# Performance work log

Measured on AMD Instinct MI355X. Metric: run time of the kernel, lower is better.

The kernel has to match this reference:

```python
import jax, jax.numpy as jnp
import numpy as np

B, S, D_IN, D_OUT = 4, 4096, 768, 768

def setup_inputs() -> dict:
    key = jax.random.key(0)
    k1, k2, k3, k4 = jax.random.split(key, 4)
    x = jax.random.normal(k1, (B, S, D_IN), dtype=jnp.float32)
    # Stored as [d_in, d_out]; torch Linear computes x @ W.T with W [d_out, d_in],
    # which is equivalent to x @ W_here for a fresh random init.
    Wq = jax.random.normal(k2, (D_IN, D_OUT), dtype=jnp.float32) * (1.0 / np.sqrt(D_IN))
    Wk = jax.random.normal(k3, (D_IN, D_OUT), dtype=jnp.float32) * (1.0 / np.sqrt(D_IN))
    Wv = jax.random.normal(k4, (D_IN, D_OUT), dtype=jnp.float32) * (1.0 / np.sqrt(D_IN))
    return {"x": x, "Wq": Wq, "Wk": Wk, "Wv": Wv}

def reference(x, Wq, Wk, Wv):
    # x: [B, S, d_in]
    q = jnp.einsum('bsi,io->bso', x, Wq)  # [B, S, d_out]
    k = jnp.einsum('bsi,io->bso', x, Wk)
    v = jnp.einsum('bsi,io->bso', x, Wv)
    scale = 1.0 / jnp.sqrt(jnp.asarray(q.shape[-1], dtype=q.dtype))
    scores = jnp.einsum('bqd,bkd->bqk', q, k)  # [B, S, S]
    S_len = scores.shape[-1]
    causal = jnp.tril(jnp.ones((S_len, S_len), dtype=bool))  # True = keep
    scores = jnp.where(causal[None, :, :], scores, -jnp.inf)
    weights = jax.nn.softmax(scores * scale, axis=-1)
    # dropout p=0.0 -> identity
    return jnp.einsum('bqk,bkd->bqd', weights, v)
```

## Files before the change

kernel.cpp:

```cpp
#include <hip/hip_runtime.h>

typedef __attribute__((ext_vector_type(8))) short short8;
typedef __attribute__((ext_vector_type(4))) float f32x4;
typedef unsigned short u16;

#define MFMA_BF16 __builtin_amdgcn_mfma_f32_16x16x32_bf16
#define S_BARRIER()  asm volatile("s_barrier" ::: "memory")
#define WAIT_LGKM0() asm volatile("s_waitcnt lgkmcnt(0)" ::: "memory")
#define WAIT_VM(n)   asm volatile("s_waitcnt vmcnt(" #n ")" ::: "memory")

__device__ __forceinline__ u16 f2bf(float f) {
    unsigned int u = __builtin_bit_cast(unsigned int, f);
    u = (u + 0x7FFFu + ((u >> 16) & 1u)) >> 16;
    return (u16)u;
}

__device__ __forceinline__ void gl_lds16(const void* g, void* l) {
    __builtin_amdgcn_global_load_lds(
        (const __attribute__((address_space(1))) unsigned int*)g,
        (__attribute__((address_space(3))) unsigned int*)l, 16, 0, 0);
}

constexpr int D = 768;
constexpr int S = 4096;
constexpr float SCALE = 0.03608439182435161f;

__device__ __forceinline__ void tri_decode(int t, int& i, int& j) {
    i = (int)((sqrtf(8.0f * t + 1.0f) - 1.0f) * 0.5f);
    while ((i + 1) * (i + 2) / 2 <= t) ++i;
    while (i * (i + 1) / 2 > t) --i;
    j = t - i * (i + 1) / 2;
}

template<int NCH, int NT>
__device__ __forceinline__ void stageT(const u16* __restrict__ g, u16* lds, int kcol, int tid) {
    #pragma unroll
    for (int i = 0; i < NCH; ++i) {
        const int ch = i * NT + tid;
        const int row = ch >> 3, c = ch & 7;
        const int cs = c ^ (row & 7);
        gl_lds16(g + (size_t)row * 768 + kcol + cs * 8, lds + ch * 8);
    }
}
__device__ __forceinline__ short8 ldsfrag(const u16* p, int row, int ks, int lane) {
    const int cs = (ks * 4 + (lane >> 4)) ^ (row & 7);
    return *reinterpret_cast<const short8*>(p + row * 64 + cs * 8);
}

__global__ __launch_bounds__(256)
void conv_x(const float* __restrict__ x, u16* __restrict__ xb) {
    const size_t i = ((size_t)blockIdx.x * 256 + threadIdx.x) * 4;
    const float4 v = *reinterpret_cast<const float4*>(x + i);
    ushort4 o;
    o.x = f2bf(v.x); o.y = f2bf(v.y); o.z = f2bf(v.z); o.w = f2bf(v.w);
    *reinterpret_cast<ushort4*>(xb + i) = o;
}

__global__ __launch_bounds__(256)
void conv_wt(const float* __restrict__ Wq, const float* __restrict__ Wk,
             const float* __restrict__ Wv, u16* __restrict__ WT) {
    __shared__ float t[64][65];
    const int tid = threadIdx.x;
    const int k0 = blockIdx.x * 64, n0 = blockIdx.y * 64, z = blockIdx.z;
    const float* __restrict__ W = (z == 0) ? Wq : ((z == 1) ? Wk : Wv);
    #pragma unroll
    for (int i = 0; i < 4; ++i) {
        const int e = (i * 256 + tid) * 4;
        const int r = e >> 6, c = e & 63;
        const float4 v = *reinterpret_cast<const float4*>(W + (size_t)(k0 + r) * D + n0 + c);
        t[r][c] = v.x; t[r][c + 1] = v.y; t[r][c + 2] = v.z; t[r][c + 3] = v.w;
    }
    __syncthreads();
    u16* O = WT + (size_t)z * D * D;
    #pragma unroll
    for (int i = 0; i < 4; ++i) {
        const int e = (i * 256 + tid) * 4;
        const int n = e >> 6, kq = e & 63;
        ushort4 o;
        o.x = f2bf(t[kq + 0][n]); o.y = f2bf(t[kq + 1][n]);
        o.z = f2bf(t[kq + 2][n]); o.w = f2bf(t[kq + 3][n]);
        *reinterpret_cast<ushort4*>(O + (size_t)(n0 + n) * D + k0 + kq) = o;
    }
}

__global__ __launch_bounds__(256, 2)
void qkv_gemm(const u16* __restrict__ xb, const u16* __restrict__ WT,
              u16* __restrict__ qo, u16* __restrict__ ko, u16* __restrict__ vt)
{
    __shared__ u16 smem[40960];
    u16* sAb = smem;
    u16* sBb = smem + 16384;
    const int tid = threadIdx.x, lane = tid & 63, w = tid >> 6;
    const int wr = w >> 1, wn = w & 1;
    const int bm = blockIdx.x * 128;
    const u16* __restrict__ A = xb + (size_t)bm * 768;
    const u16* __restrict__ B = WT + (size_t)blockIdx.y * 192 * 768;

    f32x4 acc[4][6] = {};

    stageT<4,256>(A, sAb, 0, tid);          stageT<6,256>(B, sBb, 0, tid);
    stageT<4,256>(A, sAb + 8192, 64, tid);  stageT<6,256>(B, sBb + 12288, 64, tid);
    WAIT_VM(10); S_BARRIER();

    #pragma unroll 2
    for (int kt = 0; kt < 12; ++kt) {
        const int cur = kt & 1;
        const u16* pA = sAb + cur * 8192;
        const u16* pB = sBb + cur * 12288;
        short8 a0[4], b0[6], a1[4], b1[6];
        #pragma unroll
        for (int fr = 0; fr < 4; ++fr) a0[fr] = ldsfrag(pA, wr * 64 + fr * 16 + (lane & 15), 0, lane);
        #pragma unroll
        for (int fc = 0; fc < 6; ++fc) b0[fc] = ldsfrag(pB, wn * 96 + fc * 16 + (lane & 15), 0, lane);
        #pragma unroll
        for (int fr = 0; fr < 4; ++fr)
            #pragma unroll
            for (int fc = 0; fc < 6; ++fc)
                acc[fr][fc] = MFMA_BF16(a0[fr], b0[fc], acc[fr][fc], 0, 0, 0);
        #pragma unroll
        for (int fr = 0; fr < 4; ++fr) a1[fr] = ldsfrag(pA, wr * 64 + fr * 16 + (lane & 15), 1, lane);
        #pragma unroll
        for (int fc = 0; fc < 6; ++fc) b1[fc] = ldsfrag(pB, wn * 96 + fc * 16 + (lane & 15), 1, lane);
        WAIT_LGKM0(); S_BARRIER();
        if (kt < 10) { stageT<4,256>(A, sAb + cur * 8192, (kt + 2) * 64, tid);
                       stageT<6,256>(B, sBb + cur * 12288, (kt + 2) * 64, tid); }
        __builtin_amdgcn_s_setprio(1);
        #pragma unroll
        for (int fr = 0; fr < 4; ++fr)
            #pragma unroll
            for (int fc = 0; fc < 6; ++fc)
                acc[fr][fc] = MFMA_BF16(a1[fr], b1[fc], acc[fr][fc], 0, 0, 0);
        __builtin_amdgcn_s_setprio(0);
        if (kt < 10) { WAIT_VM(10); } else { WAIT_VM(0); }
        S_BARRIER();
    }

    const int z = blockIdx.y >> 2, nb = (blockIdx.y & 3) * 192;
    if (z == 2) {
        u16* sT = smem;
        #pragma unroll
        for (int fr = 0; fr < 4; ++fr)
            #pragma unroll
            for (int fc = 0; fc < 6; ++fc) {
                const int n  = wn * 96 + fc * 16 + (lane & 15);
                const int mb = wr * 64 + fr * 16 + (lane >> 4) * 4;
                ushort4 pk;
                pk.x = f2bf(acc[fr][fc][0]); pk.y = f2bf(acc[fr][fc][1]);
                pk.z = f2bf(acc[fr][fc][2]); pk.w = f2bf(acc[fr][fc][3]);
                *reinterpret_cast<ushort4*>(&sT[n * 128 + (mb ^ ((n & 7) << 3))]) = pk;
            }
        __syncthreads();
        const int batch = bm >> 12, s_in = bm & 4095;
        u16* __restrict__ vdst = vt + ((size_t)batch * 768 + nb) * 4096 + s_in;
        #pragma unroll
        for (int v = 0; v < 12; ++v) {
            const int ch = v * 256 + tid;
            const int dd = ch >> 4, sc = ch & 15;
            const short8 o = *reinterpret_cast<const short8*>(
                &sT[dd * 128 + ((sc * 8) ^ ((dd & 7) << 3))]);
            *reinterpret_cast<short8*>(vdst + (size_t)dd * 4096 + sc * 8) = o;
        }
    } else {
        u16* __restrict__ dst = (z == 0) ? qo : ko;
        #pragma unroll
        for (int fr = 0; fr < 4; ++fr)
            #pragma unroll
            for (int fc = 0; fc < 6; ++fc)
                #pragma unroll
                for (int r = 0; r < 4; ++r) {
                    const int m = bm + wr * 64 + fr * 16 + (lane >> 4) * 4 + r;
                    const int n = nb + wn * 96 + fc * 16 + (lane & 15);
                    dst[(size_t)m * 768 + n] = f2bf(acc[fr][fc][r]);
                }
    }
}

__global__ __launch_bounds__(256, 2)
void qkt_gemm(const u16* __restrict__ Qg, const u16* __restrict__ Kg,
              u16* __restrict__ Pp, float* __restrict__ Lp)
{
    __shared__ u16 smem[32768];
    const int tid = threadIdx.x, lane = tid & 63, w = tid >> 6;
    const int wr = w >> 1, wn = w & 1;
    const int bx = blockIdx.x;
    const int bxs = (bx & 7) * 66 + (bx >> 3);
    int ti, tj;
    tri_decode(bxs, ti, tj);
    const int b = blockIdx.y;
    const u16* __restrict__ A = Qg + ((size_t)b * S + ti * 128) * 768;
    const u16* __restrict__ B = Kg + ((size_t)b * S + tj * 128) * 768;

    f32x4 acc[4][4] = {};

    stageT<4,256>(A, smem, 0, tid);           stageT<4,256>(B, smem + 16384, 0, tid);
    stageT<4,256>(A, smem + 8192, 64, tid);   stageT<4,256>(B, smem + 24576, 64, tid);
    WAIT_VM(8); S_BARRIER();

    #pragma unroll 2
    for (int kt = 0; kt < 12; ++kt) {
        const int cur = kt & 1;
        const u16* pA = smem + cur * 8192;
        const u16* pB = smem + 16384 + cur * 8192;
        short8 a0[4], b0[4], a1[4], b1[4];
        #pragma unroll
        for (int fr = 0; fr < 4; ++fr) a0[fr] = ldsfrag(pA, wr * 64 + fr * 16 + (lane & 15), 0, lane);
        #pragma unroll
        for (int fc = 0; fc < 4; ++fc) b0[fc] = ldsfrag(pB, wn * 64 + fc * 16 + (lane & 15), 0, lane);
        #pragma unroll
        for (int fr = 0; fr < 4; ++fr)
            #pragma unroll
            for (int fc = 0; fc < 4; ++fc)
                acc[fr][fc] = MFMA_BF16(a0[fr], b0[fc], acc[fr][fc], 0, 0, 0);
        #pragma unroll
        for (int fr = 0; fr < 4; ++fr) a1[fr] = ldsfrag(pA, wr * 64 + fr * 16 + (lane & 15), 1, lane);
        #pragma unroll
        for (int fc = 0; fc < 4; ++fc) b1[fc] = ldsfrag(pB, wn * 64 + fc * 16 + (lane & 15), 1, lane);
        WAIT_LGKM0(); S_BARRIER();
        if (kt < 10) { stageT<4,256>(A, smem + cur * 8192, (kt + 2) * 64, tid);
                       stageT<4,256>(B, smem + 16384 + cur * 8192, (kt + 2) * 64, tid); }
        __builtin_amdgcn_s_setprio(1);
        #pragma unroll
        for (int fr = 0; fr < 4; ++fr)
            #pragma unroll
            for (int fc = 0; fc < 4; ++fc)
                acc[fr][fc] = MFMA_BF16(a1[fr], b1[fc], acc[fr][fc], 0, 0, 0);
        __builtin_amdgcn_s_setprio(0);
        if (kt < 10) { WAIT_VM(8); } else { WAIT_VM(0); }
        S_BARRIER();
    }

    u16* sC = smem;
    const bool diag = (ti == tj);
    #pragma unroll
    for (int fr = 0; fr < 4; ++fr)
        #pragma unroll
        for (int r = 0; r < 4; ++r) {
            const int ml = wr * 64 + fr * 16 + (lane >> 4) * 4 + r;
            const int gm = ti * 128 + ml;
            float rs = 0.0f;
            #pragma unroll
            for (int fc = 0; fc < 4; ++fc) {
                const int nl = wn * 64 + fc * 16 + (lane & 15);
                float p = __expf(acc[fr][fc][r] * SCALE - 10.0f);
                if (diag && (tj * 128 + nl) > gm) p = 0.0f;
                rs += p;
                sC[ml * 132 + nl] = f2bf(p);
            }
            rs += __shfl_xor(rs, 1);
            rs += __shfl_xor(rs, 2);
            rs += __shfl_xor(rs, 4);
            rs += __shfl_xor(rs, 8);
            if ((lane & 15) == 0)
                Lp[((size_t)b * 64 + tj * 2 + wn) * 4096 + gm] = rs;
        }
    __syncthreads();
    u16* __restrict__ tbase = Pp + ((size_t)b * 528 + (size_t)ti * (ti + 1) / 2 + tj) * 16384;
    #pragma unroll
    for (int v = 0; v < 8; ++v) {
        const int ch = v * 256 + tid;
        const int row = ch >> 4, c = ch & 15;
        const short8 o = *reinterpret_cast<const short8*>(&sC[row * 132 + c * 8]);
        *reinterpret_cast<short8*>(tbase + row * 128 + c * 8) = o;
    }
}

__global__ __launch_bounds__(256)
void reduce_l(const float* __restrict__ Lp, float* __restrict__ Li)
{
    const int row = blockIdx.x * 256 + threadIdx.x;
    const int b = row >> 12, r = row & 4095;
    const int jm = 2 * (r >> 7) + 1;
    float l = 0.0f;
    for (int j = 0; j <= jm; ++j)
        l += Lp[((size_t)b * 64 + j) * 4096 + r];
    Li[row] = 1.0f / l;
}

__global__ __launch_bounds__(256)
void pv_gemm(const u16* __restrict__ Pp, const u16* __restrict__ Vt,
             const float* __restrict__ Li, float* __restrict__ out)
{
    __shared__ u16 sV[2][192 * 64];
    __shared__ u16 sP[2][128 * 64];
    const int tid  = threadIdx.x;
    const int lane = tid & 63;
    const int wd   = tid >> 6;
    const int bid  = blockIdx.x;
    const int rank = (bid < 256) ? bid : 767 - bid;
    const int i    = rank >> 4;
    const int b    = (rank >> 2) & 3;
    const int dq   = rank & 3;
    const int q0   = i * 128, d0 = dq * 192;
    const int nkt  = 2 * i + 2;
    const u16* __restrict__ Pt  = Pp + ((size_t)b * 528 + (size_t)i * (i + 1) / 2) * 16384;
    const u16* __restrict__ vtb = Vt + ((size_t)b * D + d0) * S;

    f32x4 acc[8][3] = {};

    auto stage_v = [&](int buf, int kt) {
        #pragma unroll
        for (int n = 0; n < 6; ++n) {
            const int ch  = n * 256 + tid;
            const int row = ch >> 3;
            const int csw = (ch & 7) ^ (row & 7);
            gl_lds16(vtb + (size_t)row * S + kt * 64 + csw * 8, &sV[buf][ch * 8]);
        }
    };
    auto stage_p = [&](int buf, int kt) {
        const u16* base = Pt + (size_t)(kt >> 1) * 16384 + (kt & 1) * 64;
        #pragma unroll
        for (int n = 0; n < 4; ++n) {
            const int ch  = n * 256 + tid;
            const int row = ch >> 3;
            const int csw = (ch & 7) ^ (row & 7);
            gl_lds16(base + row * 128 + csw * 8, &sP[buf][ch * 8]);
        }
    };

    stage_v(0, 0); stage_p(0, 0);
    __syncthreads();
    int cur = 0;
    for (int kt = 0; kt < nkt; ++kt) {
        if (kt + 1 < nkt) { stage_v(cur ^ 1, kt + 1); stage_p(cur ^ 1, kt + 1); }
        #pragma unroll
        for (int ks = 0; ks < 2; ++ks) {
            short8 a[8];
            #pragma unroll
            for (int fr = 0; fr < 8; ++fr) {
                const int row = fr * 16 + (lane & 15);
                const int cch = (ks * 4 + (lane >> 4)) ^ (row & 7);
                a[fr] = *reinterpret_cast<const short8*>(&sP[cur][row * 64 + cch * 8]);
            }
            #pragma unroll
            for (int fc = 0; fc < 3; ++fc) {
                const int dr  = wd * 48 + fc * 16 + (lane & 15);
                const int vch = (ks * 4 + (lane >> 4)) ^ (dr & 7);
                const short8 bv = *reinterpret_cast<const short8*>(&sV[cur][dr * 64 + vch * 8]);
                #pragma unroll
                for (int fr = 0; fr < 8; ++fr)
                    acc[fr][fc] = MFMA_BF16(a[fr], bv, acc[fr][fc], 0, 0, 0);
            }
        }
        __syncthreads();
        cur ^= 1;
    }

    #pragma unroll
    for (int fr = 0; fr < 8; ++fr)
        #pragma unroll
        for (int rr = 0; rr < 4; ++rr) {
            const int row = q0 + fr * 16 + (lane >> 4) * 4 + rr;
            const float linv = Li[b * 4096 + row];
            #pragma unroll
            for (int fc = 0; fc < 3; ++fc) {
                const int col = d0 + wd * 48 + fc * 16 + (lane & 15);
                out[((size_t)b * S + row) * D + col] = acc[fr][fc][rr] * linv;
            }
        }
}

extern "C" void kernel_launch(void* const* d_in, const int* in_sizes, int n_in,
                              void* d_out, int out_size, void* d_ws, size_t ws_size,
                              hipStream_t stream) {
    const float* x  = (const float*)d_in[0];
    const float* Wq = (const float*)d_in[1];
    const float* Wk = (const float*)d_in[2];
    const float* Wv = (const float*)d_in[3];
    float* out = (float*)d_out;

    const size_t SD = (size_t)16384 * 768;
    u16* q  = (u16*)d_ws;
    u16* k  = q  + SD;
    u16* vt = k  + SD;
    u16* xb = vt + SD;
    u16* WT = xb + SD;
    u16* Pp = WT + (size_t)3 * 768 * 768;
    float* Lp = (float*)(Pp + (size_t)4 * 528 * 16384);
    float* Li = Lp + (size_t)4 * 64 * 4096;
    (void)in_sizes; (void)n_in; (void)out_size; (void)ws_size;

    conv_x  <<<12288, 256, 0, stream>>>(x, xb);
    conv_wt <<<dim3(12, 12, 3), 256, 0, stream>>>(Wq, Wk, Wv, WT);
    qkv_gemm<<<dim3(128, 12), 256, 0, stream>>>(xb, WT, q, k, vt);
    qkt_gemm<<<dim3(528, 4), 256, 0, stream>>>(q, k, Pp, Lp);
    reduce_l<<<64, 256, 0, stream>>>(Lp, Li);
    pv_gemm <<<512, 256, 0, stream>>>(Pp, vt, Li, out);
}
```

Before: 252.9 us.

## Shrink GEMM K-tiles to 32 and N-tile to 128 for higher occupancy

The qkv and qk^T GEMMs now stage 32-wide K slices instead of 64-wide ones, using a new XOR swizzle. qkv_gemm also drops from 128x192 to 128x128 output tiles, with an 18-column grid. LDS use per block falls to about 32 KB, and launch bounds rise to 4 blocks per CU, aiming to improve latency hiding and occupancy. In exchange there are twice as many K iterations, each carrying barrier and wait overhead, less MFMA work per sync, and more redundant A-tile loads in qkv.

```diff
diff --git a/kernel.cpp b/kernel.cpp
--- a/kernel.cpp
+++ b/kernel.cpp
@@ -32,19 +32,18 @@
     j = t - i * (i + 1) / 2;
 }
 
-template<int NCH, int NT>
-__device__ __forceinline__ void stageT(const u16* __restrict__ g, u16* lds, int kcol, int tid) {
-    #pragma unroll
-    for (int i = 0; i < NCH; ++i) {
-        const int ch = i * NT + tid;
-        const int row = ch >> 3, c = ch & 7;
-        const int cs = c ^ (row & 7);
+__device__ __forceinline__ void stage32(const u16* __restrict__ g, u16* lds, int kcol, int tid) {
+    #pragma unroll
+    for (int i = 0; i < 2; ++i) {
+        const int ch = i * 256 + tid;
+        const int row = ch >> 2, c = ch & 3;
+        const int cs = c ^ (row & 3) ^ ((row >> 2) & 3);
         gl_lds16(g + (size_t)row * 768 + kcol + cs * 8, lds + ch * 8);
     }
 }
-__device__ __forceinline__ short8 ldsfrag(const u16* p, int row, int ks, int lane) {
-    const int cs = (ks * 4 + (lane >> 4)) ^ (row & 7);
-    return *reinterpret_cast<const short8*>(p + row * 64 + cs * 8);
+__device__ __forceinline__ short8 ldsfrag32(const u16* p, int row, int lane) {
+    const int pc = (lane >> 4) ^ (row & 3) ^ ((row >> 2) & 3);
+    return *reinterpret_cast<const short8*>(p + row * 32 + pc * 8);
 }
 
 __global__ __launch_bounds__(256)
@@ -83,66 +82,56 @@
     }
 }
 
-__global__ __launch_bounds__(256, 2)
+__global__ __launch_bounds__(256, 4)
 void qkv_gemm(const u16* __restrict__ xb, const u16* __restrict__ WT,
               u16* __restrict__ qo, u16* __restrict__ ko, u16* __restrict__ vt)
 {
-    __shared__ u16 smem[40960];
-    u16* sAb = smem;
-    u16* sBb = smem + 16384;
+    __shared__ u16 smem[16384];
     const int tid = threadIdx.x, lane = tid & 63, w = tid >> 6;
     const int wr = w >> 1, wn = w & 1;
     const int bm = blockIdx.x * 128;
     const u16* __restrict__ A = xb + (size_t)bm * 768;
-    const u16* __restrict__ B = WT + (size_t)blockIdx.y * 192 * 768;
-
-    f32x4 acc[4][6] = {};
-
-    stageT<4,256>(A, sAb, 0, tid);          stageT<6,256>(B, sBb, 0, tid);
-    stageT<4,256>(A, sAb + 8192, 64, tid);  stageT<6,256>(B, sBb + 12288, 64, tid);
-    WAIT_VM(10); S_BARRIER();
+    const u16* __restrict__ B = WT + (size_t)blockIdx.y * 128 * 768;
+
+    f32x4 acc[4][4] = {};
+
+    stage32(A, smem, 0, tid);          stage32(B, smem + 8192, 0, tid);
+    stage32(A, smem + 4096, 32, tid);  stage32(B, smem + 12288, 32, tid);
+    WAIT_VM(4); S_BARRIER();
 
     #pragma unroll 2
-    for (int kt = 0; kt < 12; ++kt) {
+    for (int kt = 0; kt < 24; ++kt) {
         const int cur = kt & 1;
-        const u16* pA = sAb + cur * 8192;
-        const u16* pB = sBb + cur * 12288;
-        short8 a0[4], b0[6], a1[4], b1[6];
-        #pragma unroll
-        for (int fr = 0; fr < 4; ++fr) a0[fr] = ldsfrag(pA, wr * 64 + fr * 16 + (lane & 15), 0, lane);
-        #pragma unroll
-        for (int fc = 0; fc < 6; ++fc) b0[fc] = ldsfrag(pB, wn * 96 + fc * 16 + (lane & 15), 0, lane);
+        const u16* pA = smem + cur * 4096;
+        const u16* pB = smem + 8192 + cur * 4096;
+        short8 a[4], bb[4];
+        #pragma unroll
+        for (int fr = 0; fr < 4; ++fr) a[fr] = ldsfrag32(pA, wr * 64 + fr * 16 + (lane & 15), lane);
+        #pragma unroll
+        for (int fc = 0; fc < 4; ++fc) bb[fc] = ldsfrag32(pB, wn * 64 + fc * 16 + (lane & 15), lane);
+        WAIT_LGKM0(); S_BARRIER();
+        if (kt < 22) { stage32(A, smem + cur * 4096, (kt + 2) * 32, tid);
+                       stage32(B, smem + 8192 + cur * 4096, (kt + 2) * 32, tid); }
+        __builtin_amdgcn_s_setprio(1);
         #pragma unroll
         for (int fr = 0; fr < 4; ++fr)
             #pragma unroll
-            for (int fc = 0; fc < 6; ++fc)
-                acc[fr][fc] = MFMA_BF16(a0[fr], b0[fc], acc[fr][fc], 0, 0, 0);
-        #pragma unroll
-        for (int fr = 0; fr < 4; ++fr) a1[fr] = ldsfrag(pA, wr * 64 + fr * 16 + (lane & 15), 1, lane);
-        #pragma unroll
-        for (int fc = 0; fc < 6; ++fc) b1[fc] = ldsfrag(pB, wn * 96 + fc * 16 + (lane & 15), 1, lane);
-        WAIT_LGKM0(); S_BARRIER();
-        if (kt < 10) { stageT<4,256>(A, sAb + cur * 8192, (kt + 2) * 64, tid);
-                       stageT<6,256>(B, sBb + cur * 12288, (kt + 2) * 64, tid); }
-        __builtin_amdgcn_s_setprio(1);
-        #pragma unroll
-        for (int fr = 0; fr < 4; ++fr)
-            #pragma unroll
-            for (int fc = 0; fc < 6; ++fc)
-                acc[fr][fc] = MFMA_BF16(a1[fr], b1[fc], acc[fr][fc], 0, 0, 0);
+            for (int fc = 0; fc < 4; ++fc)
+                acc[fr][fc] = MFMA_BF16(a[fr], bb[fc], acc[fr][fc], 0, 0, 0);
         __builtin_amdgcn_s_setprio(0);
-        if (kt < 10) { WAIT_VM(10); } else { WAIT_VM(0); }
+        if (kt < 22) { WAIT_VM(4); } else { WAIT_VM(0); }
         S_BARRIER();
     }
 
-    const int z = blockIdx.y >> 2, nb = (blockIdx.y & 3) * 192;
+    const int nb = blockIdx.y * 128;
+    const int z = nb / 768, nloc = nb % 768;
     if (z == 2) {
         u16* sT = smem;
         #pragma unroll
         for (int fr = 0; fr < 4; ++fr)
             #pragma unroll
-            for (int fc = 0; fc < 6; ++fc) {
-                const int n  = wn * 96 + fc * 16 + (lane & 15);
+            for (int fc = 0; fc < 4; ++fc) {
+                const int n  = wn * 64 + fc * 16 + (lane & 15);
                 const int mb = wr * 64 + fr * 16 + (lane >> 4) * 4;
                 ushort4 pk;
                 pk.x = f2bf(acc[fr][fc][0]); pk.y = f2bf(acc[fr][fc][1]);
@@ -151,9 +140,9 @@
             }
         __syncthreads();
         const int batch = bm >> 12, s_in = bm & 4095;
-        u16* __restrict__ vdst = vt + ((size_t)batch * 768 + nb) * 4096 + s_in;
-        #pragma unroll
-        for (int v = 0; v < 12; ++v) {
+        u16* __restrict__ vdst = vt + ((size_t)batch * 768 + nloc) * 4096 + s_in;
+        #pragma unroll
+        for (int v = 0; v < 8; ++v) {
             const int ch = v * 256 + tid;
             const int dd = ch >> 4, sc = ch & 15;
             const short8 o = *reinterpret_cast<const short8*>(
@@ -165,21 +154,21 @@
         #pragma unroll
         for (int fr = 0; fr < 4; ++fr)
             #pragma unroll
-            for (int fc = 0; fc < 6; ++fc)
+            for (int fc = 0; fc < 4; ++fc)
                 #pragma unroll
                 for (int r = 0; r < 4; ++r) {
                     const int m = bm + wr * 64 + fr * 16 + (lane >> 4) * 4 + r;
-                    const int n = nb + wn * 96 + fc * 16 + (lane & 15);
+                    const int n = nloc + wn * 64 + fc * 16 + (lane & 15);
                     dst[(size_t)m * 768 + n] = f2bf(acc[fr][fc][r]);
                 }
     }
 }
 
-__global__ __launch_bounds__(256, 2)
+__global__ __launch_bounds__(256, 4)
 void qkt_gemm(const u16* __restrict__ Qg, const u16* __restrict__ Kg,
               u16* __restrict__ Pp, float* __restrict__ Lp)
 {
-    __shared__ u16 smem[32768];
+    __shared__ u16 smem[16896];
     const int tid = threadIdx.x, lane = tid & 63, w = tid >> 6;
     const int wr = w >> 1, wn = w & 1;
     const int bx = blockIdx.x;
@@ -192,40 +181,31 @@
 
     f32x4 acc[4][4] = {};
 
-    stageT<4,256>(A, smem, 0, tid);           stageT<4,256>(B, smem + 16384, 0, tid);
-    stageT<4,256>(A, smem + 8192, 64, tid);   stageT<4,256>(B, smem + 24576, 64, tid);
-    WAIT_VM(8); S_BARRIER();
+    stage32(A, smem, 0, tid);          stage32(B, smem + 8192, 0, tid);
+    stage32(A, smem + 4096, 32, tid);  stage32(B, smem + 12288, 32, tid);
+    WAIT_VM(4); S_BARRIER();
 
     #pragma unroll 2
-    for (int kt = 0; kt < 12; ++kt) {
+    for (int kt = 0; kt < 24; ++kt) {
         const int cur = kt & 1;
-        const u16* pA = smem + cur * 8192;
-        const u16* pB = smem + 16384 + cur * 8192;
-        short8 a0[4], b0[4], a1[4], b1[4];
-        #pragma unroll
-        for (int fr = 0; fr < 4; ++fr) a0[fr] = ldsfrag(pA, wr * 64 + fr * 16 + (lane & 15), 0, lane);
-        #pragma unroll
-        for (int fc = 0; fc < 4; ++fc) b0[fc] = ldsfrag(pB, wn * 64 + fc * 16 + (lane & 15), 0, lane);
+        const u16* pA = smem + cur * 4096;
+        const u16* pB = smem + 8192 + cur * 4096;
+        short8 a[4], bb[4];
+        #pragma unroll
+        for (int fr = 0; fr < 4; ++fr) a[fr] = ldsfrag32(pA, wr * 64 + fr * 16 + (lane & 15), lane);
+        #pragma unroll
+        for (int fc = 0; fc < 4; ++fc) bb[fc] = ldsfrag32(pB, wn * 64 + fc * 16 + (lane & 15), lane);
+        WAIT_LGKM0(); S_BARRIER();
+        if (kt < 22) { stage32(A, smem + cur * 4096, (kt + 2) * 32, tid);
+                       stage32(B, smem + 8192 + cur * 4096, (kt + 2) * 32, tid); }
+        __builtin_amdgcn_s_setprio(1);
         #pragma unroll
         for (int fr = 0; fr < 4; ++fr)
             #pragma unroll
             for (int fc = 0; fc < 4; ++fc)
-                acc[fr][fc] = MFMA_BF16(a0[fr], b0[fc], acc[fr][fc], 0, 0, 0);
-        #pragma unroll
-        for (int fr = 0; fr < 4; ++fr) a1[fr] = ldsfrag(pA, wr * 64 + fr * 16 + (lane & 15), 1, lane);
-        #pragma unroll
-        for (int fc = 0; fc < 4; ++fc) b1[fc] = ldsfrag(pB, wn * 64 + fc * 16 + (lane & 15), 1, lane);
-        WAIT_LGKM0(); S_BARRIER();
-        if (kt < 10) { stageT<4,256>(A, smem + cur * 8192, (kt + 2) * 64, tid);
-                       stageT<4,256>(B, smem + 16384 + cur * 8192, (kt + 2) * 64, tid); }
-        __builtin_amdgcn_s_setprio(1);
-        #pragma unroll
-        for (int fr = 0; fr < 4; ++fr)
-            #pragma unroll
-            for (int fc = 0; fc < 4; ++fc)
-                acc[fr][fc] = MFMA_BF16(a1[fr], b1[fc], acc[fr][fc], 0, 0, 0);
+                acc[fr][fc] = MFMA_BF16(a[fr], bb[fc], acc[fr][fc], 0, 0, 0);
         __builtin_amdgcn_s_setprio(0);
-        if (kt < 10) { WAIT_VM(8); } else { WAIT_VM(0); }
+        if (kt < 22) { WAIT_VM(4); } else { WAIT_VM(0); }
         S_BARRIER();
     }
 
@@ -381,7 +361,7 @@
 
     conv_x  <<<12288, 256, 0, stream>>>(x, xb);
     conv_wt <<<dim3(12, 12, 3), 256, 0, stream>>>(Wq, Wk, Wv, WT);
-    qkv_gemm<<<dim3(128, 12), 256, 0, stream>>>(xb, WT, q, k, vt);
+    qkv_gemm<<<dim3(128, 18), 256, 0, stream>>>(xb, WT, q, k, vt);
     qkt_gemm<<<dim3(528, 4), 256, 0, stream>>>(q, k, Pp, Lp);
     reduce_l<<<64, 256, 0, stream>>>(Lp, Li);
     pv_gemm <<<512, 256, 0, stream>>>(Pp, vt, Li, out);
```

Result: slower. 269.2 us (+6.5%).
